# Performance work log

Hardware: AMD Instinct MI355X
Metric: run time of the kernel (lower is better)

The kernel has to match this reference:

```python
import jax, jax.numpy as jnp
import numpy as np

B, S, H = 4096, 10, 512
D_IN = 2 * H  # persona_input = 2*utterance_hidden


def _gru_cell(x, h, w_ih, w_hh, b_ih, b_hh):
    # PyTorch GRU cell math. x:[B,D_IN], h:[B,H], w_ih:[3H,D_IN], w_hh:[3H,H]
    gx = x @ w_ih.T + b_ih
    gh = h @ w_hh.T + b_hh
    xr, xz, xn = jnp.split(gx, 3, axis=-1)
    hr, hz, hn = jnp.split(gh, 3, axis=-1)
    r = jax.nn.sigmoid(xr + hr)
    z = jax.nn.sigmoid(xz + hz)
    n = jnp.tanh(xn + r * hn)
    return (1.0 - z) * n + z * h


def _run(xs, masks, hx, wif, whf, bif, bhf, wib, whb, bib, bhb):
    # xs:[B,S,D_IN], masks:[B,S] int. Single-timestep calls to a bidirectional
    # GRU: both direction cells see the same timestep, each with its own
    # carried hidden, both reset to hx[dir] where mask != 1.
    hx0 = jnp.broadcast_to(hx[0], (xs.shape[0], H))
    hx1 = jnp.broadcast_to(hx[1], (xs.shape[0], H))

    def step(carry, inp):
        hf, hb = carry
        x_t, m_t = inp
        m = (m_t == 1)[:, None]
        hf_u = jnp.where(m, hf, hx0)
        hb_u = jnp.where(m, hb, hx1)
        hf2 = _gru_cell(x_t, hf_u, wif, whf, bif, bhf)
        hb2 = _gru_cell(x_t, hb_u, wib, whb, bib, bhb)
        return (hf2, hb2), jnp.concatenate([hf2, hb2], axis=-1)

    xs_t = jnp.swapaxes(xs, 0, 1)        # [S,B,D_IN]
    ms_t = jnp.swapaxes(masks, 0, 1)     # [S,B]
    _, outs = jax.lax.scan(step, (hx0, hx1), (xs_t, ms_t))
    return jnp.swapaxes(outs, 0, 1)      # [B,S,2H]


def setup_inputs() -> dict:
    key = jax.random.key(0)
    ks = jax.random.split(key, 12)
    s = 1.0 / np.sqrt(H)
    inp = {
        "batch_sequences": jax.random.normal(ks[0], (B, S, D_IN), dtype=jnp.float32),
        "sequencemask_fr": jax.random.randint(ks[1], (B, S), 0, 2, dtype=jnp.int32),
        "sequencemask_bk": jax.random.randint(ks[2], (B, S), 0, 2, dtype=jnp.int32),
        "hx": jax.random.normal(ks[3], (2, 1, H), dtype=jnp.float32),
        "w_ih_f": jax.random.uniform(ks[4], (3 * H, D_IN), minval=-s, maxval=s, dtype=jnp.float32),
        "w_hh_f": jax.random.uniform(ks[5], (3 * H, H), minval=-s, maxval=s, dtype=jnp.float32),
        "b_ih_f": jax.random.uniform(ks[6], (3 * H,), minval=-s, maxval=s, dtype=jnp.float32),
        "b_hh_f": jax.random.uniform(ks[7], (3 * H,), minval=-s, maxval=s, dtype=jnp.float32),
        "w_ih_b": jax.random.uniform(ks[8], (3 * H, D_IN), minval=-s, maxval=s, dtype=jnp.float32),
        "w_hh_b": jax.random.uniform(ks[9], (3 * H, H), minval=-s, maxval=s, dtype=jnp.float32),
        "b_ih_b": jax.random.uniform(ks[10], (3 * H,), minval=-s, maxval=s, dtype=jnp.float32),
        "b_hh_b": jax.random.uniform(ks[11], (3 * H,), minval=-s, maxval=s, dtype=jnp.float32),
    }
    return inp


def reference(batch_sequences, sequencemask_fr, sequencemask_bk, hx,
              w_ih_f, w_hh_f, b_ih_f, b_hh_f, w_ih_b, w_hh_b, b_ih_b, b_hh_b):
    fwd = _run(batch_sequences, sequencemask_fr, hx,
               w_ih_f, w_hh_f, b_ih_f, b_hh_f, w_ih_b, w_hh_b, b_ih_b, b_hh_b)
    bwd = _run(batch_sequences[:, ::-1], sequencemask_bk, hx,
               w_ih_f, w_hh_f, b_ih_f, b_hh_f, w_ih_b, w_hh_b, b_ih_b, b_hh_b)
    bwd = bwd[:, ::-1]  # flip back to original time order
    return jnp.concatenate([fwd, bwd], axis=-1)  # [B,S,4H]
```

## Files before the change

### kernel.cpp

```cpp
#include <hip/hip_runtime.h>
#include <hip/hip_bf16.h>

#define BB   4096
#define SS   10
#define HH   512
#define DIN  1024
#define NG   1536
#define MROWS 40960

typedef __bf16 bf16x8 __attribute__((ext_vector_type(8)));
typedef __bf16 bf16x4 __attribute__((ext_vector_type(4)));
typedef float  f32x4  __attribute__((ext_vector_type(4)));

#define MFMA16(a, b, c) __builtin_amdgcn_mfma_f32_16x16x32_bf16((a), (b), (c), 0, 0, 0)

constexpr size_t SZ_GX   = (size_t)MROWS * NG * 2;
constexpr size_t OFF_GXF = 0;
constexpr size_t OFF_GXB = SZ_GX;
constexpr size_t OFF_XB  = 2 * SZ_GX;
constexpr size_t SZ_XB   = (size_t)MROWS * DIN * 2;
constexpr size_t OFF_WIHF = OFF_XB + SZ_XB;
constexpr size_t SZ_WIH  = (size_t)NG * DIN * 2;
constexpr size_t OFF_WIHB = OFF_WIHF + SZ_WIH;
constexpr size_t OFF_WHHF = OFF_WIHB + SZ_WIH;
constexpr size_t SZ_WHH  = (size_t)NG * HH * 2;
constexpr size_t OFF_WHHB = OFF_WHHF + SZ_WHH;
constexpr size_t OFF_END  = OFF_WHHB + SZ_WHH;

__device__ __forceinline__ void load_lds16(const void* g, void* l) {
    __builtin_amdgcn_global_load_lds(
        (const __attribute__((address_space(1))) void*)g,
        (__attribute__((address_space(3))) void*)l, 16, 0, 0);
}

__global__ __launch_bounds__(256) void cast_bf16_8(
    const float* __restrict__ src, __bf16* __restrict__ dst, long n)
{
    long i = ((long)blockIdx.x * 256 + threadIdx.x) * 8;
    if (i >= n) return;
    float4 v0 = *(const float4*)&src[i];
    float4 v1 = *(const float4*)&src[i + 4];
    bf16x8 o = { (__bf16)v0.x, (__bf16)v0.y, (__bf16)v0.z, (__bf16)v0.w,
                 (__bf16)v1.x, (__bf16)v1.y, (__bf16)v1.z, (__bf16)v1.w };
    *(bf16x8*)&dst[i] = o;
}

__global__ __launch_bounds__(256) void input_gemm(
    const __bf16* __restrict__ Xb,
    const __bf16* __restrict__ Wf, const __bf16* __restrict__ Wb,
    const float* __restrict__ biasf, const float* __restrict__ biasb,
    __bf16* __restrict__ gxf, __bf16* __restrict__ gxb)
{
    __shared__ __bf16 smA[128 * 64];
    __shared__ __bf16 smB[128 * 64];

    const int set = blockIdx.z;
    const __bf16* W   = set ? Wb : Wf;
    const float* bias = set ? biasb : biasf;
    __bf16* gx        = set ? gxb : gxf;

    const int n0 = blockIdx.x * 128;
    const int m0 = blockIdx.y * 128;
    const int tid  = threadIdx.x;
    const int lane = tid & 63;
    const int wid  = tid >> 6;
    const int lm   = lane & 15;
    const int quad = lane >> 4;
    const int m_base = (wid & 1) * 64;
    const int n_base = (wid >> 1) * 64;
    const int srow   = tid >> 3;
    const int schunk = (tid & 7) * 8;

    f32x4 acc[4][4] = {};

    for (int kt = 0; kt < 16; ++kt) {
        const int k0 = kt * 64;
        __syncthreads();
#pragma unroll
        for (int ra = 0; ra < 4; ++ra) {
            int row = ra * 32 + srow;
            load_lds16(&Xb[(size_t)(m0 + row) * DIN + k0 + schunk],
                       &smA[row * 64 + schunk]);
        }
#pragma unroll
        for (int ra = 0; ra < 4; ++ra) {
            int row = ra * 32 + srow;
            load_lds16(&W[(size_t)(n0 + row) * DIN + k0 + schunk],
                       &smB[row * 64 + schunk]);
        }
        __syncthreads();
#pragma unroll
        for (int kk = 0; kk < 2; ++kk) {
            const int kof = kk * 32 + quad * 8;
            bf16x8 a[4], b[4];
#pragma unroll
            for (int mt = 0; mt < 4; ++mt)
                a[mt] = *(const bf16x8*)&smA[(m_base + mt * 16 + lm) * 64 + kof];
#pragma unroll
            for (int nt = 0; nt < 4; ++nt)
                b[nt] = *(const bf16x8*)&smB[(n_base + nt * 16 + lm) * 64 + kof];
#pragma unroll
            for (int mt = 0; mt < 4; ++mt)
#pragma unroll
                for (int nt = 0; nt < 4; ++nt)
                    acc[mt][nt] = MFMA16(a[mt], b[nt], acc[mt][nt]);
        }
    }

#pragma unroll
    for (int mt = 0; mt < 4; ++mt) {
#pragma unroll
        for (int nt = 0; nt < 4; ++nt) {
            const int col = n0 + n_base + nt * 16 + lm;
            const float bv = bias[col];
#pragma unroll
            for (int r = 0; r < 4; ++r) {
                const int row = m0 + m_base + mt * 16 + quad * 4 + r;
                gx[(size_t)row * NG + col] = (__bf16)(acc[mt][nt][r] + bv);
            }
        }
    }
}

__global__ __launch_bounds__(512) void gru_rec(
    const __bf16* __restrict__ whhf, const __bf16* __restrict__ whhb,
    const float* __restrict__ bhhf, const float* __restrict__ bhhb,
    const __bf16* __restrict__ gxf, const __bf16* __restrict__ gxb,
    const int* __restrict__ mfr, const int* __restrict__ mbk,
    const float* __restrict__ hx, float* out)
{
    __shared__ __bf16 hbuf[64 * 512];

    const int bx = blockIdx.x;
    const int stream = bx & 3;
    const int b0 = (bx >> 2) * 64;
    const int set = stream & 1;
    const int dir = stream >> 1;

    const __bf16* whh = set ? whhb : whhf;
    const float* bhh  = set ? bhhb : bhhf;
    const __bf16* gx  = set ? gxb : gxf;
    const int* mask   = dir ? mbk : mfr;
    const float* hx0  = hx + set * HH;
    const int ocol0   = stream * HH;

    const int tid  = threadIdx.x;
    const int lane = tid & 63;
    const int wid  = tid >> 6;
    const int lm   = lane & 15;
    const int quad = lane >> 4;
    const int wcol0 = wid * 64;

    const int brow = tid >> 3;
    const int bc0  = (tid & 7) * 64;

    for (int i = 0; i < 10; ++i) {
        const int t = dir ? (9 - i) : i;

        {
            const int m = mask[(size_t)(b0 + brow) * SS + i];
            const bool reset = (i == 0) || (m != 1);
            const float* src;
            if (reset) {
                src = &hx0[bc0];
            } else {
                const int tp = dir ? (10 - i) : (i - 1);
                src = &out[((size_t)(b0 + brow) * SS + tp) * (4 * HH) + ocol0 + bc0];
            }
#pragma unroll
            for (int c = 0; c < 64; c += 4) {
                float4 v = *(const float4*)&src[c];
                bf16x4 b4 = { (__bf16)v.x, (__bf16)v.y, (__bf16)v.z, (__bf16)v.w };
                *(bf16x4*)&hbuf[brow * 512 + bc0 + c] = b4;
            }
        }
        __syncthreads();

        for (int jt = 0; jt < 4; ++jt) {
            const int jc = wcol0 + jt * 16;
            const __bf16* wr = whh + (size_t)(jc + lm) * HH;
            f32x4 acc[4][3] = {};
#pragma unroll 4
            for (int kk = 0; kk < 16; ++kk) {
                const int k = kk * 32 + quad * 8;
                bf16x8 a0 = *(const bf16x8*)&hbuf[(lm)      * 512 + k];
                bf16x8 a1 = *(const bf16x8*)&hbuf[(16 + lm) * 512 + k];
                bf16x8 a2 = *(const bf16x8*)&hbuf[(32 + lm) * 512 + k];
                bf16x8 a3 = *(const bf16x8*)&hbuf[(48 + lm) * 512 + k];
                bf16x8 br = *(const bf16x8*)&wr[k];
                bf16x8 bz = *(const bf16x8*)&wr[(size_t)512 * HH + k];
                bf16x8 bn = *(const bf16x8*)&wr[(size_t)1024 * HH + k];
                acc[0][0] = MFMA16(a0, br, acc[0][0]);
                acc[1][0] = MFMA16(a1, br, acc[1][0]);
                acc[2][0] = MFMA16(a2, br, acc[2][0]);
                acc[3][0] = MFMA16(a3, br, acc[3][0]);
                acc[0][1] = MFMA16(a0, bz, acc[0][1]);
                acc[1][1] = MFMA16(a1, bz, acc[1][1]);
                acc[2][1] = MFMA16(a2, bz, acc[2][1]);
                acc[3][1] = MFMA16(a3, bz, acc[3][1]);
                acc[0][2] = MFMA16(a0, bn, acc[0][2]);
                acc[1][2] = MFMA16(a1, bn, acc[1][2]);
                acc[2][2] = MFMA16(a2, bn, acc[2][2]);
                acc[3][2] = MFMA16(a3, bn, acc[3][2]);
            }

            const int col = jc + lm;
            const float bhr = bhh[col];
            const float bhz = bhh[HH + col];
            const float bhn = bhh[2 * HH + col];
#pragma unroll
            for (int mt = 0; mt < 4; ++mt) {
#pragma unroll
                for (int r = 0; r < 4; ++r) {
                    const int row = mt * 16 + quad * 4 + r;
                    const int b = b0 + row;
                    const size_t gi = ((size_t)b * SS + t) * NG + col;
                    const float gxr = (float)gx[gi];
                    const float gxz = (float)gx[gi + HH];
                    const float gxn = (float)gx[gi + 2 * HH];
                    const float ghr = acc[mt][0][r] + bhr;
                    const float ghz = acc[mt][1][r] + bhz;
                    const float ghn = acc[mt][2][r] + bhn;
                    const float rg = 1.0f / (1.0f + __expf(-(gxr + ghr)));
                    const float zg = 1.0f / (1.0f + __expf(-(gxz + ghz)));
                    const float ng = tanhf(gxn + rg * ghn);
                    const float hu = (float)hbuf[row * 512 + col];
                    const float hn = (1.0f - zg) * ng + zg * hu;
                    out[((size_t)b * SS + t) * (4 * HH) + ocol0 + col] = hn;
                }
            }
        }
        __syncthreads();
    }
}

extern "C" void kernel_launch(void* const* d_in, const int* in_sizes, int n_in,
                              void* d_out, int out_size, void* d_ws, size_t ws_size,
                              hipStream_t stream)
{
    (void)in_sizes; (void)n_in; (void)out_size;
    if (ws_size < OFF_END) return;

    const float* X    = (const float*)d_in[0];
    const int*   mfr  = (const int*)d_in[1];
    const int*   mbk  = (const int*)d_in[2];
    const float* hx   = (const float*)d_in[3];
    const float* wihf = (const float*)d_in[4];
    const float* whhf = (const float*)d_in[5];
    const float* bihf = (const float*)d_in[6];
    const float* bhhf = (const float*)d_in[7];
    const float* wihb = (const float*)d_in[8];
    const float* whhb = (const float*)d_in[9];
    const float* bihb = (const float*)d_in[10];
    const float* bhhb = (const float*)d_in[11];
    float* out = (float*)d_out;
    char*  ws  = (char*)d_ws;

    __bf16* gxf = (__bf16*)(ws + OFF_GXF);
    __bf16* gxb = (__bf16*)(ws + OFF_GXB);
    __bf16* Xb  = (__bf16*)(ws + OFF_XB);
    __bf16* Wif = (__bf16*)(ws + OFF_WIHF);
    __bf16* Wib = (__bf16*)(ws + OFF_WIHB);
    __bf16* Whf = (__bf16*)(ws + OFF_WHHF);
    __bf16* Whb = (__bf16*)(ws + OFF_WHHB);

    cast_bf16_8<<<20480, 256, 0, stream>>>(X,    Xb,  (long)MROWS * DIN);
    cast_bf16_8<<<768,   256, 0, stream>>>(wihf, Wif, (long)NG * DIN);
    cast_bf16_8<<<768,   256, 0, stream>>>(wihb, Wib, (long)NG * DIN);
    cast_bf16_8<<<384,   256, 0, stream>>>(whhf, Whf, (long)NG * HH);
    cast_bf16_8<<<384,   256, 0, stream>>>(whhb, Whb, (long)NG * HH);

    input_gemm<<<dim3(12, 320, 2), 256, 0, stream>>>(Xb, Wif, Wib, bihf, bihb, gxf, gxb);

    gru_rec<<<256, 512, 0, stream>>>(Whf, Whb, bhhf, bhhb, gxf, gxb, mfr, mbk, hx, out);
}
```

Before: 1.616 ms.

## Keep GRU hidden state in LDS across steps, swizzle it, stage GEMM epilogue

The recurrent kernel no longer reloads the previous hidden state from the global output buffer each timestep. Instead each thread keeps its new hidden values in registers and writes them, masked against hx, straight back into an XOR-swizzled LDS buffer, which is meant to avoid bank conflicts on the MFMA operand reads. The input GEMM epilogue now stages bf16 results through shared memory so it can write coalesced 16-byte rows instead of scattered 2-byte stores. The costs are extra register pressure from hreg (64 bf16 per thread), an extra barrier per step, and the next-step mask loads.

```diff
diff --git a/kernel.cpp b/kernel.cpp
--- a/kernel.cpp
+++ b/kernel.cpp
@@ -13,6 +13,8 @@
 typedef float  f32x4  __attribute__((ext_vector_type(4)));
 
 #define MFMA16(a, b, c) __builtin_amdgcn_mfma_f32_16x16x32_bf16((a), (b), (c), 0, 0, 0)
+
+#define HIDX(r, c) (((r) * 512) + ((((c) >> 3) ^ ((r) & 7)) << 3) + ((c) & 7))
 
 constexpr size_t SZ_GX   = (size_t)MROWS * NG * 2;
 constexpr size_t OFF_GXF = 0;
@@ -51,8 +53,7 @@
     const float* __restrict__ biasf, const float* __restrict__ biasb,
     __bf16* __restrict__ gxf, __bf16* __restrict__ gxb)
 {
-    __shared__ __bf16 smA[128 * 64];
-    __shared__ __bf16 smB[128 * 64];
+    __shared__ __bf16 sm[17408];
 
     const int set = blockIdx.z;
     const __bf16* W   = set ? Wb : Wf;
@@ -71,6 +72,9 @@
     const int srow   = tid >> 3;
     const int schunk = (tid & 7) * 8;
 
+    __bf16* smA = sm;
+    __bf16* smB = sm + 8192;
+
     f32x4 acc[4][4] = {};
 
     for (int kt = 0; kt < 16; ++kt) {
@@ -107,18 +111,30 @@
         }
     }
 
+    __syncthreads();
 #pragma unroll
     for (int mt = 0; mt < 4; ++mt) {
 #pragma unroll
         for (int nt = 0; nt < 4; ++nt) {
-            const int col = n0 + n_base + nt * 16 + lm;
-            const float bv = bias[col];
+            const int colL = n_base + nt * 16 + lm;
+            const float bv = bias[n0 + colL];
 #pragma unroll
             for (int r = 0; r < 4; ++r) {
-                const int row = m0 + m_base + mt * 16 + quad * 4 + r;
-                gx[(size_t)row * NG + col] = (__bf16)(acc[mt][nt][r] + bv);
+                const int rowL = m_base + mt * 16 + quad * 4 + r;
+                sm[rowL * 136 + colL] = (__bf16)(acc[mt][nt][r] + bv);
             }
         }
+    }
+    __syncthreads();
+#pragma unroll
+    for (int p = 0; p < 4; ++p) {
+        const int rowL = p * 32 + (tid >> 3);
+        const int c0 = (tid & 7) * 16;
+        bf16x8 v0 = *(const bf16x8*)&sm[rowL * 136 + c0];
+        bf16x8 v1 = *(const bf16x8*)&sm[rowL * 136 + c0 + 8];
+        __bf16* dst = &gx[(size_t)(m0 + rowL) * NG + n0 + c0];
+        *(bf16x8*)dst = v0;
+        *(bf16x8*)(dst + 8) = v1;
     }
 }
 
@@ -151,42 +167,35 @@
     const int quad = lane >> 4;
     const int wcol0 = wid * 64;
 
-    const int brow = tid >> 3;
-    const int bc0  = (tid & 7) * 64;
+    {
+        const int brow = tid >> 3;
+        const int bc0  = (tid & 7) * 64;
+#pragma unroll
+        for (int c = 0; c < 64; c += 4) {
+            float4 v = *(const float4*)&hx0[bc0 + c];
+            bf16x4 b4 = { (__bf16)v.x, (__bf16)v.y, (__bf16)v.z, (__bf16)v.w };
+            *(bf16x4*)&hbuf[HIDX(brow, bc0 + c)] = b4;
+        }
+    }
+    __syncthreads();
 
     for (int i = 0; i < 10; ++i) {
         const int t = dir ? (9 - i) : i;
-
-        {
-            const int m = mask[(size_t)(b0 + brow) * SS + i];
-            const bool reset = (i == 0) || (m != 1);
-            const float* src;
-            if (reset) {
-                src = &hx0[bc0];
-            } else {
-                const int tp = dir ? (10 - i) : (i - 1);
-                src = &out[((size_t)(b0 + brow) * SS + tp) * (4 * HH) + ocol0 + bc0];
-            }
-#pragma unroll
-            for (int c = 0; c < 64; c += 4) {
-                float4 v = *(const float4*)&src[c];
-                bf16x4 b4 = { (__bf16)v.x, (__bf16)v.y, (__bf16)v.z, (__bf16)v.w };
-                *(bf16x4*)&hbuf[brow * 512 + bc0 + c] = b4;
-            }
-        }
-        __syncthreads();
-
+        __bf16 hreg[4][16];
+
+#pragma unroll
         for (int jt = 0; jt < 4; ++jt) {
             const int jc = wcol0 + jt * 16;
             const __bf16* wr = whh + (size_t)(jc + lm) * HH;
             f32x4 acc[4][3] = {};
 #pragma unroll 4
             for (int kk = 0; kk < 16; ++kk) {
+                const int koff = (((kk * 4 + quad) ^ (lm & 7)) << 3);
                 const int k = kk * 32 + quad * 8;
-                bf16x8 a0 = *(const bf16x8*)&hbuf[(lm)      * 512 + k];
-                bf16x8 a1 = *(const bf16x8*)&hbuf[(16 + lm) * 512 + k];
-                bf16x8 a2 = *(const bf16x8*)&hbuf[(32 + lm) * 512 + k];
-                bf16x8 a3 = *(const bf16x8*)&hbuf[(48 + lm) * 512 + k];
+                bf16x8 a0 = *(const bf16x8*)&hbuf[(lm)      * 512 + koff];
+                bf16x8 a1 = *(const bf16x8*)&hbuf[(16 + lm) * 512 + koff];
+                bf16x8 a2 = *(const bf16x8*)&hbuf[(32 + lm) * 512 + koff];
+                bf16x8 a3 = *(const bf16x8*)&hbuf[(48 + lm) * 512 + koff];
                 bf16x8 br = *(const bf16x8*)&wr[k];
                 bf16x8 bz = *(const bf16x8*)&wr[(size_t)512 * HH + k];
                 bf16x8 bn = *(const bf16x8*)&wr[(size_t)1024 * HH + k];
@@ -224,10 +233,38 @@
                     const float rg = 1.0f / (1.0f + __expf(-(gxr + ghr)));
                     const float zg = 1.0f / (1.0f + __expf(-(gxz + ghz)));
                     const float ng = tanhf(gxn + rg * ghn);
-                    const float hu = (float)hbuf[row * 512 + col];
+                    const float hu = (float)hbuf[HIDX(row, col)];
                     const float hn = (1.0f - zg) * ng + zg * hu;
                     out[((size_t)b * SS + t) * (4 * HH) + ocol0 + col] = hn;
+                    hreg[jt][mt * 4 + r] = (__bf16)hn;
                 }
+            }
+        }
+
+        bool keep[4][4];
+        if (i < 9) {
+#pragma unroll
+            for (int mt = 0; mt < 4; ++mt)
+#pragma unroll
+                for (int r = 0; r < 4; ++r)
+                    keep[mt][r] =
+                        (mask[(size_t)(b0 + mt * 16 + quad * 4 + r) * SS + (i + 1)] == 1);
+        }
+
+        __syncthreads();
+
+        if (i < 9) {
+#pragma unroll
+            for (int jt = 0; jt < 4; ++jt) {
+                const int col = wcol0 + jt * 16 + lm;
+                const __bf16 hxb = (__bf16)hx0[col];
+#pragma unroll
+                for (int mt = 0; mt < 4; ++mt)
+#pragma unroll
+                    for (int r = 0; r < 4; ++r) {
+                        const int row = mt * 16 + quad * 4 + r;
+                        hbuf[HIDX(row, col)] = keep[mt][r] ? hreg[jt][mt * 4 + r] : hxb;
+                    }
             }
         }
         __syncthreads();
```

Result: slower. 2.326 ms (+43.9%).
